# Kernel tuning notes

Hardware: AMD Instinct MI355X
Metric: run time of the kernel (lower is better)

## Reference

```python
import jax, jax.numpy as jnp
import numpy as np

N_PATCHES = 131072
MAX_LEN = 8
D_LOCAL = 64
N_HEADS = 2
D_K = D_LOCAL // N_HEADS  # 32
D_FF = 2 * D_LOCAL       # 128
D_MODEL = 128
VOCAB = 258
EPS = float(np.finfo(np.float32).eps)  # torch RMSNorm default eps


def setup_inputs() -> dict:
    key = jax.random.key(0)
    ks = jax.random.split(key, 12)
    s = 0.05
    return {
        "tokens": jax.random.randint(ks[0], (N_PATCHES, MAX_LEN), 0, VOCAB, dtype=jnp.int32),
        "lengths": jax.random.randint(ks[1], (N_PATCHES,), 1, MAX_LEN + 1, dtype=jnp.int32),
        "emb": jax.random.normal(ks[2], (VOCAB, D_LOCAL), jnp.float32) * s,
        "qkv_w": jax.random.normal(ks[3], (D_LOCAL, 3 * D_LOCAL), jnp.float32) * s,
        "w_o": jax.random.normal(ks[4], (D_LOCAL, D_LOCAL), jnp.float32) * s,
        "norm1_w": jnp.ones((D_LOCAL,), jnp.float32),
        "norm2_w": jnp.ones((D_LOCAL,), jnp.float32),
        "ffn_w1": jax.random.normal(ks[5], (D_LOCAL, D_FF), jnp.float32) * s,
        "ffn_w2": jax.random.normal(ks[6], (D_FF, D_LOCAL), jnp.float32) * s,
        "norm_w": jnp.ones((D_LOCAL,), jnp.float32),
        "proj_w": jax.random.normal(ks[7], (D_LOCAL, D_MODEL), jnp.float32) * s,
        "proj_b": jnp.zeros((D_MODEL,), jnp.float32),
    }


def _rms_norm(x, w):
    return x * jax.lax.rsqrt(jnp.mean(x * x, axis=-1, keepdims=True) + EPS) * w


def _rope_tables(seq_len):
    half = D_K // 2
    freq = (1.0 / 10000.0) ** jnp.linspace(0.0, 1.0, half, dtype=jnp.float32)
    theta = jnp.arange(seq_len, dtype=jnp.float32)[:, None] * freq  # [L, half]
    return jnp.cos(theta), jnp.sin(theta)


def _rope(x, cos, sin):
    # x: [N, H, L, D_K]; cos/sin: [L, D_K//2]
    x1, x2 = jnp.split(x, 2, axis=-1)
    return jnp.concatenate([x1 * cos - x2 * sin, x1 * sin + x2 * cos], axis=-1)


def reference(tokens, lengths, emb, qkv_w, w_o, norm1_w, norm2_w,
              ffn_w1, ffn_w2, norm_w, proj_w, proj_b):
    N, L = tokens.shape
    x = emb[tokens]  # [N, L, D_LOCAL]

    # --- attention sublayer ---
    xn = _rms_norm(x, norm1_w)
    qkv = (xn @ qkv_w).reshape(N, L, 3, N_HEADS, D_K)
    qkv = jnp.transpose(qkv, (2, 0, 3, 1, 4))  # [3, N, H, L, D_K]
    q, k, v = qkv[0], qkv[1], qkv[2]
    cos, sin = _rope_tables(L)
    q = _rope(q, cos, sin)
    k = _rope(k, cos, sin)
    scores = jnp.einsum('nhqd,nhkd->nhqk', q, k) / jnp.sqrt(jnp.float32(D_K))
    causal = jnp.tril(jnp.ones((L, L), bool))
    scores = jnp.where(causal, scores, jnp.float32(-1e30))
    attn = jax.nn.softmax(scores, axis=-1)
    out = jnp.einsum('nhqk,nhkd->nhqd', attn, v)
    out = jnp.transpose(out, (0, 2, 1, 3)).reshape(N, L, D_LOCAL)
    x = x + out @ w_o

    # --- FFN sublayer (SiLU MLP) ---
    h = _rms_norm(x, norm2_w)
    x = x + jax.nn.silu(h @ ffn_w1) @ ffn_w2

    # --- final norm + masked mean pool (causal attn => pads don't leak) ---
    x = _rms_norm(x, norm_w)
    mask = (jnp.arange(L)[None, :] < lengths[:, None]).astype(x.dtype)  # [N, L]
    pooled = jnp.sum(x * mask[:, :, None], axis=1) / lengths[:, None].astype(x.dtype)

    patch_emb = pooled @ proj_w + proj_b  # [N, D_MODEL]
    return patch_emb[None, :, :]  # [1, N, D_MODEL] as in torch (cat + unsqueeze(0))
```

## Files before the change

### kernel.cpp

```cpp
#include <hip/hip_runtime.h>
#include <math.h>

#define NP 131072

typedef unsigned short u16;
typedef __bf16 v8bf __attribute__((ext_vector_type(8)));
typedef unsigned v4u __attribute__((ext_vector_type(4)));
typedef float v4f __attribute__((ext_vector_type(4)));

#define MFMA(a, b, c) __builtin_amdgcn_mfma_f32_16x16x32_bf16(a, b, c, 0, 0, 0)
#define EPS 1.1920928955078125e-07f

__device__ __forceinline__ u16 f2b(float f) { return __builtin_bit_cast(u16, (__bf16)f); }
__device__ __forceinline__ unsigned f2b2(float a, float b) {
    return (unsigned)f2b(a) | ((unsigned)f2b(b) << 16);
}
__device__ __forceinline__ float frcp(float x) { return __builtin_amdgcn_rcpf(x); }
__device__ __forceinline__ float frsq(float x) { return __builtin_amdgcn_rsqf(x); }
__device__ __forceinline__ v8bf ldfrag(const u16* p) { return *(const v8bf*)p; }
__device__ __forceinline__ v8bf zfrag() { v4u z = {0,0,0,0}; return __builtin_bit_cast(v8bf, z); }

__global__ void prep_weights(const float* __restrict__ qkvw, const float* __restrict__ wo,
                             const float* __restrict__ w1, const float* __restrict__ w2,
                             const float* __restrict__ pw, u16* __restrict__ wt) {
    int i = blockIdx.x * 256 + threadIdx.x;
    if (i < 12288)      { int n = i >> 6, k = i & 63;                wt[i] = f2b(qkvw[k * 192 + n]); }
    else if (i < 16384) { int j = i - 12288; int n = j >> 6, k = j & 63;  wt[i] = f2b(wo[k * 64 + n]); }
    else if (i < 24576) { int j = i - 16384; int n = j >> 6, k = j & 63;  wt[i] = f2b(w1[k * 128 + n]); }
    else if (i < 32768) { int j = i - 24576; int n = j >> 7, k = j & 127; wt[i] = f2b(w2[k * 64 + n]); }
    else if (i < 40960) { int j = i - 32768; int n = j >> 6, k = j & 63;  wt[i] = f2b(pw[k * 128 + n]); }
}

#define QA 0
#define KA 9216
#define SHA 0
#define PO 18432
#define SMEM_U16 19456

__global__ __launch_bounds__(256, 4)
void enc_mfma(const int* __restrict__ tokens, const int* __restrict__ lengths,
              const float* __restrict__ emb,
              const float* __restrict__ n1w, const float* __restrict__ n2w,
              const float* __restrict__ nw, const float* __restrict__ pb,
              const u16* __restrict__ wt, float* __restrict__ out) {
    __shared__ __align__(16) u16 s16[SMEM_U16];

    const int tid = threadIdx.x;
    const int l   = tid & 63;
    const int wv  = tid >> 6;
    const int lr  = l & 15;
    const int lk  = l >> 4;
    const int p0  = blockIdx.x << 4;

    {
        const int r = tid >> 1, hh = tid & 1;
        const int tok = tokens[p0 * 8 + r];
        const float* er = emb + (size_t)tok * 64 + hh * 32;
        float xv[32];
        #pragma unroll
        for (int i = 0; i < 8; ++i) {
            float4 f = ((const float4*)er)[i];
            xv[4*i] = f.x; xv[4*i+1] = f.y; xv[4*i+2] = f.z; xv[4*i+3] = f.w;
        }
        float ss = 0.f;
        #pragma unroll
        for (int k = 0; k < 32; ++k) ss = fmaf(xv[k], xv[k], ss);
        ss += __shfl_xor(ss, 1);
        const float rstd = frsq(ss * 0.015625f + EPS);
        const int key = r & 7;
        #pragma unroll
        for (int k = 0; k < 16; ++k) {
            const float a = xv[2*k]     * n1w[hh*32 + 2*k]     * rstd;
            const float b = xv[2*k + 1] * n1w[hh*32 + 2*k + 1] * rstd;
            const int addr = QA + r * 72 + (((hh*4 + (k >> 2)) ^ key) << 3) + ((2*k) & 7);
            *(unsigned*)(s16 + addr) = f2b2(a, b);
        }
    }

    float csr[4], snr[4];
    {
        const float fr = exp2f((float)lr * (-13.287712379549449f / 15.f));
        #pragma unroll
        for (int r = 0; r < 4; ++r) {
            const float th = (float)((lk*4 + r) & 7) * fr;
            csr[r] = __cosf(th); snr[r] = __sinf(th);
        }
    }

    unsigned vpx[4][2], vpy[4][2];

    {
        v8bf afr[2][2];
        #pragma unroll
        for (int mi = 0; mi < 2; ++mi)
            #pragma unroll
            for (int ks = 0; ks < 2; ++ks)
                afr[mi][ks] = ldfrag(s16 + QA + (wv*32 + mi*16 + lr) * 72
                                     + (((ks*4 + lk) ^ (lr & 7)) << 3));

        #pragma unroll
        for (int j = 0; j < 4; ++j) {
            v8bf blo[2], bhi[2];
            #pragma unroll
            for (int ks = 0; ks < 2; ++ks) {
                blo[ks] = ldfrag(wt + ((2*j)     * 16 + lr) * 64 + ks*32 + lk*8);
                bhi[ks] = ldfrag(wt + ((2*j + 1) * 16 + lr) * 64 + ks*32 + lk*8);
            }
            const int isq = (j < 2) ? 1 : 0;
            const int head = isq ? j : (j - 2);
            const int dst = isq ? QA : KA;
            #pragma unroll
            for (int mi = 0; mi < 2; ++mi) {
                v4f lo = {0.f,0.f,0.f,0.f}, hi = {0.f,0.f,0.f,0.f};
                #pragma unroll
                for (int ks = 0; ks < 2; ++ks) {
                    lo = MFMA(afr[mi][ks], blo[ks], lo);
                    hi = MFMA(afr[mi][ks], bhi[ks], hi);
                }
                #pragma unroll
                for (int r = 0; r < 4; ++r) {
                    const float c = csr[r], s = snr[r];
                    float nlo = lo[r] * c - hi[r] * s;
                    float nhi = lo[r] * s + hi[r] * c;
                    if (isq) { nlo *= 0.17677669529663687f; nhi *= 0.17677669529663687f; }
                    const int row = wv*32 + mi*16 + lk*4 + r;
                    *(unsigned*)(s16 + dst + row*72 + head*32 + 2*lr) = f2b2(nlo, nhi);
                }
            }
        }
        #pragma unroll
        for (int ntl = 0; ntl < 4; ++ntl) {
            v8bf b[2];
            #pragma unroll
            for (int ks = 0; ks < 2; ++ks)
                b[ks] = ldfrag(wt + ((8 + ntl) * 16 + lr) * 64 + ks*32 + lk*8);
            #pragma unroll
            for (int mi = 0; mi < 2; ++mi) {
                v4f ac = {0.f,0.f,0.f,0.f};
                #pragma unroll
                for (int ks = 0; ks < 2; ++ks) ac = MFMA(afr[mi][ks], b[ks], ac);
                vpx[ntl][mi] = f2b2(ac[0], ac[1]);
                vpy[ntl][mi] = f2b2(ac[2], ac[3]);
            }
        }
    }

    const int pbase = QA + wv * 2304;
    float rsum[4][4];
    {
        v8bf aq[4], bk[4];
        #pragma unroll
        for (int uu = 0; uu < 4; ++uu) {
            const int h = uu >> 1, g = 2*wv + (uu & 1);
            aq[uu] = ldfrag(s16 + QA + (g*16 + lr)*72 + h*32 + lk*8);
            bk[uu] = ldfrag(s16 + KA + (g*16 + lr)*72 + h*32 + lk*8);
        }
        #pragma unroll
        for (int uu = 0; uu < 4; ++uu) {
            v4f zz = {0.f,0.f,0.f,0.f};
            v4f sc = MFMA(aq[uu], bk[uu], zz);
            #pragma unroll
            for (int r = 0; r < 4; ++r) {
                const int row = lk*4 + r;
                const bool valid = ((lr >> 3) == (row >> 3)) && ((lr & 7) <= (row & 7));
                float e = valid ? __expf(sc[r]) : 0.f;
                float sum = e;
                sum += __shfl_xor(sum, 1);
                sum += __shfl_xor(sum, 2);
                sum += __shfl_xor(sum, 4);
                sum += __shfl_xor(sum, 8);
                rsum[uu][r] = frcp(sum);
                s16[pbase + uu*512 + row*32 + lr] = f2b(e);
            }
        }
    }

    {
        const int s0 = lr + ((lk & 1) << 5);
        const int s1 = s0 + 16;
        #pragma unroll
        for (int uu = 0; uu < 4; ++uu) {
            const int mw = uu & 1, g = 2*wv + mw;
            v8bf ap = zfrag();
            if (lk < 2) ap = ldfrag(s16 + pbase + uu*512 + lr*32 + lk*8);
            #pragma unroll
            for (int dl = 0; dl < 2; ++dl) {
                const int dt = (uu >> 1)*2 + dl;
                v4u bw;
                bw[0] = __shfl(vpx[dt][mw], s0);
                bw[1] = __shfl(vpy[dt][mw], s0);
                bw[2] = __shfl(vpx[dt][mw], s1);
                bw[3] = __shfl(vpy[dt][mw], s1);
                if (lk >= 2) { bw[0] = 0; bw[1] = 0; bw[2] = 0; bw[3] = 0; }
                v8bf bv = __builtin_bit_cast(v8bf, bw);
                v4f zz = {0.f,0.f,0.f,0.f};
                v4f oc = MFMA(ap, bv, zz);
                #pragma unroll
                for (int r = 0; r < 4; ++r) {
                    const int row = g*16 + lk*4 + r;
                    s16[KA + row*72 + dt*16 + lr] = f2b(oc[r] * rsum[uu][r]);
                }
            }
        }
    }

    v4f x2[2][4];
    {
        v8bf ao[2][2];
        #pragma unroll
        for (int mi = 0; mi < 2; ++mi)
            #pragma unroll
            for (int ks = 0; ks < 2; ++ks)
                ao[mi][ks] = ldfrag(s16 + KA + (wv*32 + mi*16 + lr)*72 + ks*32 + lk*8);
        int trow[2][4];
        #pragma unroll
        for (int mi = 0; mi < 2; ++mi)
            #pragma unroll
            for (int r = 0; r < 4; ++r)
                trow[mi][r] = tokens[p0*8 + wv*32 + mi*16 + lk*4 + r];
        #pragma unroll
        for (int mi = 0; mi < 2; ++mi)
            #pragma unroll
            for (int nt = 0; nt < 4; ++nt)
                #pragma unroll
                for (int r = 0; r < 4; ++r)
                    x2[mi][nt][r] = emb[(size_t)trow[mi][r] * 64 + nt*16 + lr];
        #pragma unroll
        for (int nt = 0; nt < 4; ++nt) {
            v8bf b[2];
            #pragma unroll
            for (int ks = 0; ks < 2; ++ks)
                b[ks] = ldfrag(wt + 12288 + (nt*16 + lr)*64 + ks*32 + lk*8);
            #pragma unroll
            for (int mi = 0; mi < 2; ++mi)
                #pragma unroll
                for (int ks = 0; ks < 2; ++ks)
                    x2[mi][nt] = MFMA(ao[mi][ks], b[ks], x2[mi][nt]);
        }
        #pragma unroll
        for (int mi = 0; mi < 2; ++mi) {
            float ssq[4] = {0.f,0.f,0.f,0.f};
            #pragma unroll
            for (int nt = 0; nt < 4; ++nt)
                #pragma unroll
                for (int r = 0; r < 4; ++r) ssq[r] = fmaf(x2[mi][nt][r], x2[mi][nt][r], ssq[r]);
            #pragma unroll
            for (int r = 0; r < 4; ++r) {
                ssq[r] += __shfl_xor(ssq[r], 1);
                ssq[r] += __shfl_xor(ssq[r], 2);
                ssq[r] += __shfl_xor(ssq[r], 4);
                ssq[r] += __shfl_xor(ssq[r], 8);
                ssq[r] = frsq(ssq[r] * 0.015625f + EPS);
            }
            #pragma unroll
            for (int nt = 0; nt < 4; ++nt) {
                const float nv = n2w[nt*16 + lr];
                #pragma unroll
                for (int r = 0; r < 4; ++r) {
                    const int row = wv*32 + mi*16 + lk*4 + r;
                    s16[QA + row*72 + nt*16 + lr] = f2b(x2[mi][nt][r] * nv * ssq[r]);
                }
            }
        }
    }

    {
        v8bf a[2][2];
        #pragma unroll
        for (int mi = 0; mi < 2; ++mi)
            #pragma unroll
            for (int ks = 0; ks < 2; ++ks)
                a[mi][ks] = ldfrag(s16 + QA + (wv*32 + mi*16 + lr)*72 + ks*32 + lk*8);
        __syncthreads();
        #pragma unroll
        for (int nt = 0; nt < 8; ++nt) {
            v8bf b[2];
            #pragma unroll
            for (int ks = 0; ks < 2; ++ks)
                b[ks] = ldfrag(wt + 16384 + (nt*16 + lr)*64 + ks*32 + lk*8);
            #pragma unroll
            for (int mi = 0; mi < 2; ++mi) {
                v4f hc = {0.f,0.f,0.f,0.f};
                #pragma unroll
                for (int ks = 0; ks < 2; ++ks) hc = MFMA(a[mi][ks], b[ks], hc);
                #pragma unroll
                for (int r = 0; r < 4; ++r) {
                    const float v = hc[r];
                    const float sl = v * frcp(1.f + __expf(-v));
                    const int row = wv*32 + mi*16 + lk*4 + r;
                    s16[SHA + row*136 + nt*16 + lr] = f2b(sl);
                }
            }
        }
    }

    {
        v8bf a2[2][4];
        #pragma unroll
        for (int mi = 0; mi < 2; ++mi)
            #pragma unroll
            for (int ks = 0; ks < 4; ++ks)
                a2[mi][ks] = ldfrag(s16 + SHA + (wv*32 + mi*16 + lr)*136 + ks*32 + lk*8);
        #pragma unroll
        for (int nt = 0; nt < 4; ++nt) {
            v8bf b[4];
            #pragma unroll
            for (int ks = 0; ks < 4; ++ks)
                b[ks] = ldfrag(wt + 24576 + (nt*16 + lr)*128 + ks*32 + lk*8);
            #pragma unroll
            for (int mi = 0; mi < 2; ++mi)
                #pragma unroll
                for (int ks = 0; ks < 4; ++ks)
                    x2[mi][nt] = MFMA(a2[mi][ks], b[ks], x2[mi][nt]);
        }
        #pragma unroll
        for (int mi = 0; mi < 2; ++mi) {
            float ssq[4] = {0.f,0.f,0.f,0.f};
            #pragma unroll
            for (int nt = 0; nt < 4; ++nt)
                #pragma unroll
                for (int r = 0; r < 4; ++r) ssq[r] = fmaf(x2[mi][nt][r], x2[mi][nt][r], ssq[r]);
            #pragma unroll
            for (int r = 0; r < 4; ++r) {
                ssq[r] += __shfl_xor(ssq[r], 1);
                ssq[r] += __shfl_xor(ssq[r], 2);
                ssq[r] += __shfl_xor(ssq[r], 4);
                ssq[r] += __shfl_xor(ssq[r], 8);
                ssq[r] = frsq(ssq[r] * 0.015625f + EPS);
            }
            const int lp = wv*4 + mi*2 + (lk >> 1);
            const int len = lengths[p0 + lp];
            const float invl = frcp((float)len);
            #pragma unroll
            for (int nt = 0; nt < 4; ++nt) {
                const float nv = nw[nt*16 + lr];
                float part = 0.f;
                #pragma unroll
                for (int r = 0; r < 4; ++r) {
                    const int tt = (lk & 1) * 4 + r;
                    const float xn3 = x2[mi][nt][r] * nv * ssq[r];
                    part += (tt < len) ? xn3 : 0.f;
                }
                part += __shfl_xor(part, 16);
                if ((lk & 1) == 0) {
                    const int addr = PO + lp*64
                        + (((2*nt + (lr >> 3)) ^ (lp & 7)) << 3) + (lr & 7);
                    s16[addr] = f2b(part * invl);
                }
            }
        }
    }
    __syncthreads();

    {
        v8bf ap2[2];
        #pragma unroll
        for (int ks = 0; ks < 2; ++ks)
            ap2[ks] = ldfrag(s16 + PO + lr*64 + (((ks*4 + lk) ^ (lr & 7)) << 3));
        #pragma unroll
        for (int ntl = 0; ntl < 2; ++ntl) {
            const int nt = wv*2 + ntl;
            v8bf b[2];
            #pragma unroll
            for (int ks = 0; ks < 2; ++ks)
                b[ks] = ldfrag(wt + 32768 + (nt*16 + lr)*64 + ks*32 + lk*8);
            const float bias = pb[nt*16 + lr];
            v4f ac = {bias, bias, bias, bias};
            #pragma unroll
            for (int ks = 0; ks < 2; ++ks) ac = MFMA(ap2[ks], b[ks], ac);
            #pragma unroll
            for (int r = 0; r < 4; ++r)
                out[(size_t)(p0 + lk*4 + r) * 128 + nt*16 + lr] = ac[r];
        }
    }
}

extern "C" void kernel_launch(void* const* d_in, const int* in_sizes, int n_in,
                              void* d_out, int out_size, void* d_ws, size_t ws_size,
                              hipStream_t stream) {
    const int*   tokens  = (const int*)  d_in[0];
    const int*   lengths = (const int*)  d_in[1];
    const float* emb     = (const float*)d_in[2];
    const float* qkvw    = (const float*)d_in[3];
    const float* wo      = (const float*)d_in[4];
    const float* n1w     = (const float*)d_in[5];
    const float* n2w     = (const float*)d_in[6];
    const float* w1      = (const float*)d_in[7];
    const float* w2      = (const float*)d_in[8];
    const float* nw      = (const float*)d_in[9];
    const float* pw      = (const float*)d_in[10];
    const float* pb      = (const float*)d_in[11];
    float* outp = (float*)d_out;
    u16* wt = (u16*)d_ws;

    hipLaunchKernelGGL(prep_weights, dim3(160), dim3(256), 0, stream,
                       qkvw, wo, w1, w2, pw, wt);
    hipLaunchKernelGGL(enc_mfma, dim3(NP / 16), dim3(256), 0, stream,
                       tokens, lengths, emb, n1w, n2w, nw, pb, (const u16*)wt, outp);
}
```

Measured before the change: 395.4 us.

## Process 32 patches per block with four M-tiles per wave

Each block now handles 32 patches instead of 16, so every wave processes 64 token rows (four 16-row MFMA tiles). Weight fragments loaded from global memory are reused across twice as many rows, and the FFN down-projection loop is reordered so the K-slice is outermost, reusing each B fragment across all tiles. To fit the register budget, the post-attention residual is kept as packed bf16 between sublayers, which adds rounding error to the residual stream. LDS use doubles and launch bounds drop to 2 blocks per CU, which lowers occupancy in exchange for more reuse per wave.

Measured after the change: 321.7 us. -18.6%, faster.

```diff
diff --git a/kernel.cpp b/kernel.cpp
--- a/kernel.cpp
+++ b/kernel.cpp
@@ -14,6 +14,9 @@
 __device__ __forceinline__ u16 f2b(float f) { return __builtin_bit_cast(u16, (__bf16)f); }
 __device__ __forceinline__ unsigned f2b2(float a, float b) {
     return (unsigned)f2b(a) | ((unsigned)f2b(b) << 16);
+}
+__device__ __forceinline__ float b2f(u16 u) {
+    unsigned v = (unsigned)u << 16; return __builtin_bit_cast(float, v);
 }
 __device__ __forceinline__ float frcp(float x) { return __builtin_amdgcn_rcpf(x); }
 __device__ __forceinline__ float frsq(float x) { return __builtin_amdgcn_rsqf(x); }
@@ -32,12 +35,12 @@
 }
 
 #define QA 0
-#define KA 9216
+#define KA 18432
 #define SHA 0
-#define PO 18432
-#define SMEM_U16 19456
-
-__global__ __launch_bounds__(256, 4)
+#define PO 36864
+#define SMEM_U16 38912
+
+__global__ __launch_bounds__(256, 2)
 void enc_mfma(const int* __restrict__ tokens, const int* __restrict__ lengths,
               const float* __restrict__ emb,
               const float* __restrict__ n1w, const float* __restrict__ n2w,
@@ -50,29 +53,28 @@
     const int wv  = tid >> 6;
     const int lr  = l & 15;
     const int lk  = l >> 4;
-    const int p0  = blockIdx.x << 4;
-
-    {
-        const int r = tid >> 1, hh = tid & 1;
+    const int p0  = blockIdx.x << 5;
+
+    {
+        const int r = tid;
         const int tok = tokens[p0 * 8 + r];
-        const float* er = emb + (size_t)tok * 64 + hh * 32;
-        float xv[32];
-        #pragma unroll
-        for (int i = 0; i < 8; ++i) {
+        const float* er = emb + (size_t)tok * 64;
+        float xv[64];
+        #pragma unroll
+        for (int i = 0; i < 16; ++i) {
             float4 f = ((const float4*)er)[i];
             xv[4*i] = f.x; xv[4*i+1] = f.y; xv[4*i+2] = f.z; xv[4*i+3] = f.w;
         }
         float ss = 0.f;
         #pragma unroll
-        for (int k = 0; k < 32; ++k) ss = fmaf(xv[k], xv[k], ss);
-        ss += __shfl_xor(ss, 1);
+        for (int k = 0; k < 64; ++k) ss = fmaf(xv[k], xv[k], ss);
         const float rstd = frsq(ss * 0.015625f + EPS);
         const int key = r & 7;
         #pragma unroll
-        for (int k = 0; k < 16; ++k) {
-            const float a = xv[2*k]     * n1w[hh*32 + 2*k]     * rstd;
-            const float b = xv[2*k + 1] * n1w[hh*32 + 2*k + 1] * rstd;
-            const int addr = QA + r * 72 + (((hh*4 + (k >> 2)) ^ key) << 3) + ((2*k) & 7);
+        for (int k = 0; k < 32; ++k) {
+            const float a = xv[2*k]     * n1w[2*k]     * rstd;
+            const float b = xv[2*k + 1] * n1w[2*k + 1] * rstd;
+            const int addr = QA + r * 72 + (((k >> 2) ^ key) << 3) + ((2*k) & 7);
             *(unsigned*)(s16 + addr) = f2b2(a, b);
         }
     }
@@ -87,15 +89,15 @@
         }
     }
 
-    unsigned vpx[4][2], vpy[4][2];
-
-    {
-        v8bf afr[2][2];
-        #pragma unroll
-        for (int mi = 0; mi < 2; ++mi)
-            #pragma unroll
-            for (int ks = 0; ks < 2; ++ks)
-                afr[mi][ks] = ldfrag(s16 + QA + (wv*32 + mi*16 + lr) * 72
+    unsigned vpx[4][4], vpy[4][4];
+
+    {
+        v8bf afr[4][2];
+        #pragma unroll
+        for (int mi = 0; mi < 4; ++mi)
+            #pragma unroll
+            for (int ks = 0; ks < 2; ++ks)
+                afr[mi][ks] = ldfrag(s16 + QA + (wv*64 + mi*16 + lr) * 72
                                      + (((ks*4 + lk) ^ (lr & 7)) << 3));
 
         #pragma unroll
@@ -110,7 +112,7 @@
             const int head = isq ? j : (j - 2);
             const int dst = isq ? QA : KA;
             #pragma unroll
-            for (int mi = 0; mi < 2; ++mi) {
+            for (int mi = 0; mi < 4; ++mi) {
                 v4f lo = {0.f,0.f,0.f,0.f}, hi = {0.f,0.f,0.f,0.f};
                 #pragma unroll
                 for (int ks = 0; ks < 2; ++ks) {
@@ -123,7 +125,7 @@
                     float nlo = lo[r] * c - hi[r] * s;
                     float nhi = lo[r] * s + hi[r] * c;
                     if (isq) { nlo *= 0.17677669529663687f; nhi *= 0.17677669529663687f; }
-                    const int row = wv*32 + mi*16 + lk*4 + r;
+                    const int row = wv*64 + mi*16 + lk*4 + r;
                     *(unsigned*)(s16 + dst + row*72 + head*32 + 2*lr) = f2b2(nlo, nhi);
                 }
             }
@@ -135,7 +137,7 @@
             for (int ks = 0; ks < 2; ++ks)
                 b[ks] = ldfrag(wt + ((8 + ntl) * 16 + lr) * 64 + ks*32 + lk*8);
             #pragma unroll
-            for (int mi = 0; mi < 2; ++mi) {
+            for (int mi = 0; mi < 4; ++mi) {
                 v4f ac = {0.f,0.f,0.f,0.f};
                 #pragma unroll
                 for (int ks = 0; ks < 2; ++ks) ac = MFMA(afr[mi][ks], b[ks], ac);
@@ -145,20 +147,21 @@
         }
     }
 
-    const int pbase = QA + wv * 2304;
-    float rsum[4][4];
-    {
-        v8bf aq[4], bk[4];
-        #pragma unroll
-        for (int uu = 0; uu < 4; ++uu) {
-            const int h = uu >> 1, g = 2*wv + (uu & 1);
+    const int pbase = QA + wv * 4608;
+    float rsum[8][4];
+    {
+        v8bf aq[8];
+        #pragma unroll
+        for (int uu = 0; uu < 8; ++uu) {
+            const int h = uu >> 2, g = 4*wv + (uu & 3);
             aq[uu] = ldfrag(s16 + QA + (g*16 + lr)*72 + h*32 + lk*8);
-            bk[uu] = ldfrag(s16 + KA + (g*16 + lr)*72 + h*32 + lk*8);
-        }
-        #pragma unroll
-        for (int uu = 0; uu < 4; ++uu) {
+        }
+        #pragma unroll
+        for (int uu = 0; uu < 8; ++uu) {
+            const int h = uu >> 2, g = 4*wv + (uu & 3);
+            v8bf bk = ldfrag(s16 + KA + (g*16 + lr)*72 + h*32 + lk*8);
             v4f zz = {0.f,0.f,0.f,0.f};
-            v4f sc = MFMA(aq[uu], bk[uu], zz);
+            v4f sc = MFMA(aq[uu], bk, zz);
             #pragma unroll
             for (int r = 0; r < 4; ++r) {
                 const int row = lk*4 + r;
@@ -179,13 +182,13 @@
         const int s0 = lr + ((lk & 1) << 5);
         const int s1 = s0 + 16;
         #pragma unroll
-        for (int uu = 0; uu < 4; ++uu) {
-            const int mw = uu & 1, g = 2*wv + mw;
+        for (int uu = 0; uu < 8; ++uu) {
+            const int mw = uu & 3, g = 4*wv + mw;
             v8bf ap = zfrag();
             if (lk < 2) ap = ldfrag(s16 + pbase + uu*512 + lr*32 + lk*8);
             #pragma unroll
             for (int dl = 0; dl < 2; ++dl) {
-                const int dt = (uu >> 1)*2 + dl;
+                const int dt = (uu >> 2)*2 + dl;
                 v4u bw;
                 bw[0] = __shfl(vpx[dt][mw], s0);
                 bw[1] = __shfl(vpy[dt][mw], s0);
@@ -204,27 +207,27 @@
         }
     }
 
-    v4f x2[2][4];
-    {
-        v8bf ao[2][2];
-        #pragma unroll
-        for (int mi = 0; mi < 2; ++mi)
-            #pragma unroll
-            for (int ks = 0; ks < 2; ++ks)
-                ao[mi][ks] = ldfrag(s16 + KA + (wv*32 + mi*16 + lr)*72 + ks*32 + lk*8);
-        int trow[2][4];
-        #pragma unroll
-        for (int mi = 0; mi < 2; ++mi)
+    unsigned x2p[4][4][2];
+    {
+        v8bf ao[4][2];
+        #pragma unroll
+        for (int mi = 0; mi < 4; ++mi)
+            #pragma unroll
+            for (int ks = 0; ks < 2; ++ks)
+                ao[mi][ks] = ldfrag(s16 + KA + (wv*64 + mi*16 + lr)*72 + ks*32 + lk*8);
+        v4f x2[4][4];
+        #pragma unroll
+        for (int mi = 0; mi < 4; ++mi) {
+            int trow[4];
             #pragma unroll
             for (int r = 0; r < 4; ++r)
-                trow[mi][r] = tokens[p0*8 + wv*32 + mi*16 + lk*4 + r];
-        #pragma unroll
-        for (int mi = 0; mi < 2; ++mi)
+                trow[r] = tokens[p0*8 + wv*64 + mi*16 + lk*4 + r];
             #pragma unroll
             for (int nt = 0; nt < 4; ++nt)
                 #pragma unroll
                 for (int r = 0; r < 4; ++r)
-                    x2[mi][nt][r] = emb[(size_t)trow[mi][r] * 64 + nt*16 + lr];
+                    x2[mi][nt][r] = emb[(size_t)trow[r] * 64 + nt*16 + lr];
+        }
         #pragma unroll
         for (int nt = 0; nt < 4; ++nt) {
             v8bf b[2];
@@ -232,13 +235,13 @@
             for (int ks = 0; ks < 2; ++ks)
                 b[ks] = ldfrag(wt + 12288 + (nt*16 + lr)*64 + ks*32 + lk*8);
             #pragma unroll
-            for (int mi = 0; mi < 2; ++mi)
+            for (int mi = 0; mi < 4; ++mi)
                 #pragma unroll
                 for (int ks = 0; ks < 2; ++ks)
                     x2[mi][nt] = MFMA(ao[mi][ks], b[ks], x2[mi][nt]);
         }
         #pragma unroll
-        for (int mi = 0; mi < 2; ++mi) {
+        for (int mi = 0; mi < 4; ++mi) {
             float ssq[4] = {0.f,0.f,0.f,0.f};
             #pragma unroll
             for (int nt = 0; nt < 4; ++nt)
@@ -257,20 +260,22 @@
                 const float nv = n2w[nt*16 + lr];
                 #pragma unroll
                 for (int r = 0; r < 4; ++r) {
-                    const int row = wv*32 + mi*16 + lk*4 + r;
+                    const int row = wv*64 + mi*16 + lk*4 + r;
                     s16[QA + row*72 + nt*16 + lr] = f2b(x2[mi][nt][r] * nv * ssq[r]);
                 }
-            }
-        }
-    }
-
-    {
-        v8bf a[2][2];
-        #pragma unroll
-        for (int mi = 0; mi < 2; ++mi)
-            #pragma unroll
-            for (int ks = 0; ks < 2; ++ks)
-                a[mi][ks] = ldfrag(s16 + QA + (wv*32 + mi*16 + lr)*72 + ks*32 + lk*8);
+                x2p[mi][nt][0] = f2b2(x2[mi][nt][0], x2[mi][nt][1]);
+                x2p[mi][nt][1] = f2b2(x2[mi][nt][2], x2[mi][nt][3]);
+            }
+        }
+    }
+
+    {
+        v8bf a[4][2];
+        #pragma unroll
+        for (int mi = 0; mi < 4; ++mi)
+            #pragma unroll
+            for (int ks = 0; ks < 2; ++ks)
+                a[mi][ks] = ldfrag(s16 + QA + (wv*64 + mi*16 + lr)*72 + ks*32 + lk*8);
         __syncthreads();
         #pragma unroll
         for (int nt = 0; nt < 8; ++nt) {
@@ -279,7 +284,7 @@
             for (int ks = 0; ks < 2; ++ks)
                 b[ks] = ldfrag(wt + 16384 + (nt*16 + lr)*64 + ks*32 + lk*8);
             #pragma unroll
-            for (int mi = 0; mi < 2; ++mi) {
+            for (int mi = 0; mi < 4; ++mi) {
                 v4f hc = {0.f,0.f,0.f,0.f};
                 #pragma unroll
                 for (int ks = 0; ks < 2; ++ks) hc = MFMA(a[mi][ks], b[ks], hc);
@@ -287,7 +292,7 @@
                 for (int r = 0; r < 4; ++r) {
                     const float v = hc[r];
                     const float sl = v * frcp(1.f + __expf(-v));
-                    const int row = wv*32 + mi*16 + lk*4 + r;
+                    const int row = wv*64 + mi*16 + lk*4 + r;
                     s16[SHA + row*136 + nt*16 + lr] = f2b(sl);
                 }
             }
@@ -295,31 +300,38 @@
     }
 
     {
-        v8bf a2[2][4];
-        #pragma unroll
-        for (int mi = 0; mi < 2; ++mi)
-            #pragma unroll
-            for (int ks = 0; ks < 4; ++ks)
-                a2[mi][ks] = ldfrag(s16 + SHA + (wv*32 + mi*16 + lr)*136 + ks*32 + lk*8);
-        #pragma unroll
-        for (int nt = 0; nt < 4; ++nt) {
-            v8bf b[4];
-            #pragma unroll
-            for (int ks = 0; ks < 4; ++ks)
-                b[ks] = ldfrag(wt + 24576 + (nt*16 + lr)*128 + ks*32 + lk*8);
-            #pragma unroll
-            for (int mi = 0; mi < 2; ++mi)
-                #pragma unroll
-                for (int ks = 0; ks < 4; ++ks)
-                    x2[mi][nt] = MFMA(a2[mi][ks], b[ks], x2[mi][nt]);
-        }
-        #pragma unroll
-        for (int mi = 0; mi < 2; ++mi) {
+        v4f acc[4][4];
+        #pragma unroll
+        for (int mi = 0; mi < 4; ++mi)
+            #pragma unroll
+            for (int nt = 0; nt < 4; ++nt) {
+                acc[mi][nt][0] = b2f((u16)(x2p[mi][nt][0] & 0xffff));
+                acc[mi][nt][1] = b2f((u16)(x2p[mi][nt][0] >> 16));
+                acc[mi][nt][2] = b2f((u16)(x2p[mi][nt][1] & 0xffff));
+                acc[mi][nt][3] = b2f((u16)(x2p[mi][nt][1] >> 16));
+            }
+        #pragma unroll
+        for (int ks = 0; ks < 4; ++ks) {
+            v8bf a2[4], bb[4];
+            #pragma unroll
+            for (int mi = 0; mi < 4; ++mi)
+                a2[mi] = ldfrag(s16 + SHA + (wv*64 + mi*16 + lr)*136 + ks*32 + lk*8);
+            #pragma unroll
+            for (int nt = 0; nt < 4; ++nt)
+                bb[nt] = ldfrag(wt + 24576 + (nt*16 + lr)*128 + ks*32 + lk*8);
+            #pragma unroll
+            for (int mi = 0; mi < 4; ++mi)
+                #pragma unroll
+                for (int nt = 0; nt < 4; ++nt)
+                    acc[mi][nt] = MFMA(a2[mi], bb[nt], acc[mi][nt]);
+        }
+        #pragma unroll
+        for (int mi = 0; mi < 4; ++mi) {
             float ssq[4] = {0.f,0.f,0.f,0.f};
             #pragma unroll
             for (int nt = 0; nt < 4; ++nt)
                 #pragma unroll
-                for (int r = 0; r < 4; ++r) ssq[r] = fmaf(x2[mi][nt][r], x2[mi][nt][r], ssq[r]);
+                for (int r = 0; r < 4; ++r) ssq[r] = fmaf(acc[mi][nt][r], acc[mi][nt][r], ssq[r]);
             #pragma unroll
             for (int r = 0; r < 4; ++r) {
                 ssq[r] += __shfl_xor(ssq[r], 1);
@@ -328,7 +340,7 @@
                 ssq[r] += __shfl_xor(ssq[r], 8);
                 ssq[r] = frsq(ssq[r] * 0.015625f + EPS);
             }
-            const int lp = wv*4 + mi*2 + (lk >> 1);
+            const int lp = wv*8 + mi*2 + (lk >> 1);
             const int len = lengths[p0 + lp];
             const float invl = frcp((float)len);
             #pragma unroll
@@ -338,7 +350,7 @@
                 #pragma unroll
                 for (int r = 0; r < 4; ++r) {
                     const int tt = (lk & 1) * 4 + r;
-                    const float xn3 = x2[mi][nt][r] * nv * ssq[r];
+                    const float xn3 = acc[mi][nt][r] * nv * ssq[r];
                     part += (tt < len) ? xn3 : 0.f;
                 }
                 part += __shfl_xor(part, 16);
@@ -353,24 +365,27 @@
     __syncthreads();
 
     {
-        v8bf ap2[2];
-        #pragma unroll
-        for (int ks = 0; ks < 2; ++ks)
-            ap2[ks] = ldfrag(s16 + PO + lr*64 + (((ks*4 + lk) ^ (lr & 7)) << 3));
-        #pragma unroll
-        for (int ntl = 0; ntl < 2; ++ntl) {
-            const int nt = wv*2 + ntl;
-            v8bf b[2];
-            #pragma unroll
-            for (int ks = 0; ks < 2; ++ks)
-                b[ks] = ldfrag(wt + 32768 + (nt*16 + lr)*64 + ks*32 + lk*8);
-            const float bias = pb[nt*16 + lr];
-            v4f ac = {bias, bias, bias, bias};
-            #pragma unroll
-            for (int ks = 0; ks < 2; ++ks) ac = MFMA(ap2[ks], b[ks], ac);
-            #pragma unroll
-            for (int r = 0; r < 4; ++r)
-                out[(size_t)(p0 + lk*4 + r) * 128 + nt*16 + lr] = ac[r];
+        #pragma unroll
+        for (int mi = 0; mi < 2; ++mi) {
+            v8bf ap2[2];
+            #pragma unroll
+            for (int ks = 0; ks < 2; ++ks)
+                ap2[ks] = ldfrag(s16 + PO + (mi*16 + lr)*64 + (((ks*4 + lk) ^ (lr & 7)) << 3));
+            #pragma unroll
+            for (int ntl = 0; ntl < 2; ++ntl) {
+                const int nt = wv*2 + ntl;
+                v8bf b[2];
+                #pragma unroll
+                for (int ks = 0; ks < 2; ++ks)
+                    b[ks] = ldfrag(wt + 32768 + (nt*16 + lr)*64 + ks*32 + lk*8);
+                const float bias = pb[nt*16 + lr];
+                v4f ac = {bias, bias, bias, bias};
+                #pragma unroll
+                for (int ks = 0; ks < 2; ++ks) ac = MFMA(ap2[ks], b[ks], ac);
+                #pragma unroll
+                for (int r = 0; r < 4; ++r)
+                    out[(size_t)(p0 + mi*16 + lk*4 + r) * 128 + nt*16 + lr] = ac[r];
+            }
         }
     }
 }
@@ -395,6 +410,6 @@
 
     hipLaunchKernelGGL(prep_weights, dim3(160), dim3(256), 0, stream,
                        qkvw, wo, w1, w2, pw, wt);
-    hipLaunchKernelGGL(enc_mfma, dim3(NP / 16), dim3(256), 0, stream,
+    hipLaunchKernelGGL(enc_mfma, dim3(NP / 32), dim3(256), 0, stream,
                        tokens, lengths, emb, n1w, n2w, nw, pb, (const u16*)wt, outp);
 }
```
